# Performance work log

Measured on AMD Instinct MI355X. Metric: run time of the kernel, lower is better.

The kernel has to match this reference:

```python
import jax, jax.numpy as jnp
import numpy as np

N = 50000
E = 800000
D_IN = 64
D_HID = 64
N_CLASS = 40


def setup_inputs() -> dict:
    key = jax.random.key(0)
    ks = jax.random.split(key, 9)
    x = jax.random.normal(ks[0], (N, D_IN), dtype=jnp.float32)
    edge_index = jax.random.randint(ks[1], (2, E), 0, N, dtype=jnp.int64)
    # GCNConv weights (glorot-ish scale) and biases
    W1 = jax.random.normal(ks[2], (D_IN, D_HID), dtype=jnp.float32) / np.sqrt(D_IN)
    b1 = jnp.zeros((D_HID,), dtype=jnp.float32)
    W2 = jax.random.normal(ks[3], (D_HID, D_HID), dtype=jnp.float32) / np.sqrt(D_HID)
    b2 = jnp.zeros((D_HID,), dtype=jnp.float32)
    Wc = jax.random.normal(ks[4], (D_HID, N_CLASS), dtype=jnp.float32) / np.sqrt(D_HID)
    bc = jnp.zeros((N_CLASS,), dtype=jnp.float32)
    return {"x": x, "edge_index": edge_index, "W1": W1, "b1": b1,
            "W2": W2, "b2": b2, "Wc": Wc, "bc": bc}


def _gcn_conv(x, W, b, src, dst, n_nodes):
    """PyG GCNConv: add self-loops, sym-normalized mean aggregation, then +bias.
    out = D^{-1/2} (A + I) D^{-1/2} X W + b
    src/dst already include self-loops."""
    h = x @ W  # [N, D_out] -- transform before aggregation (fewer FLOPs if D_out<=D_in)
    deg = jax.ops.segment_sum(jnp.ones_like(dst, dtype=h.dtype), dst, num_segments=n_nodes)
    dinv = jnp.where(deg > 0, jax.lax.rsqrt(deg), 0.0)  # [N]
    norm = dinv[src] * dinv[dst]  # [E+N]
    msg = h[src] * norm[:, None]  # gather + scale
    out = jax.ops.segment_sum(msg, dst, num_segments=n_nodes)  # scatter-add
    return out + b


def reference(x, edge_index, W1, b1, W2, b2, Wc, bc):
    n = x.shape[0]
    loops = jnp.arange(n, dtype=edge_index.dtype)
    src = jnp.concatenate([edge_index[0], loops])
    dst = jnp.concatenate([edge_index[1], loops])
    h = jnp.tanh(_gcn_conv(x, W1, b1, src, dst, n))
    h = jnp.tanh(_gcn_conv(h, W2, b2, src, dst, n))
    out = h @ Wc + bc
    return (out, h)
```

## Files before the change

kernel.cpp:

```cpp
#include <hip/hip_runtime.h>
#include <math.h>

#define NN 50000
#define NE 800000
#define D 64
#define NC 40
#define NBUCK 196
#define SLAB 16384
#define EPB 2048
#define PADROW 0xC350C350u

typedef unsigned short u16;
typedef unsigned int u32;

__device__ __forceinline__ u16 f32_to_bf16(float v) {
    u32 x = __float_as_uint(v);
    x += 0x7FFFu + ((x >> 16) & 1u);
    return (u16)(x >> 16);
}
__device__ __forceinline__ float bflo(u32 v) { return __uint_as_float(v << 16); }
__device__ __forceinline__ float bfhi(u32 v) { return __uint_as_float(v & 0xffff0000u); }


__global__ __launch_bounds__(256) void bucket_scatter(const int* __restrict__ ei,
                                                      int* __restrict__ cursor,
                                                      u32* __restrict__ slab) {
    __shared__ int sums[256];
    __shared__ int lofs[256];
    __shared__ int lcur[256];
    __shared__ int gbase[256];
    __shared__ int tot_s;
    __shared__ u32 sorted[EPB];
    __shared__ int gdest[EPB];
    int tid = threadIdx.x;

    u32 pk[8];
    int nmine = 0;
    int e0 = blockIdx.x * EPB + tid * 8;
    if (e0 < NE) {
        nmine = 8;
#pragma unroll
        for (int j = 0; j < 2; ++j) {
            int4 ss = *(const int4*)&ei[e0 + j * 4];
            int4 dd = *(const int4*)&ei[NE + e0 + j * 4];
            pk[j * 4 + 0] = ((u32)dd.x << 16) | (u32)ss.x;
            pk[j * 4 + 1] = ((u32)dd.y << 16) | (u32)ss.y;
            pk[j * 4 + 2] = ((u32)dd.z << 16) | (u32)ss.z;
            pk[j * 4 + 3] = ((u32)dd.w << 16) | (u32)ss.w;
        }
    }

    sums[tid] = 0;
    __syncthreads();
    for (int j = 0; j < nmine; ++j) atomicAdd(&sums[pk[j] >> 24], 1);
    __syncthreads();
    int v = sums[tid];
    __syncthreads();
    for (int off = 1; off < 256; off <<= 1) {
        int u = (tid >= off) ? sums[tid - off] : 0;
        __syncthreads();
        sums[tid] += u;
        __syncthreads();
    }
    lofs[tid] = sums[tid] - v;
    lcur[tid] = sums[tid] - v;
    if (tid == 255) tot_s = sums[255];
    if (tid < NBUCK) gbase[tid] = atomicAdd(&cursor[tid], v);
    __syncthreads();

    for (int j = 0; j < nmine; ++j) {
        u32 p = pk[j];
        int bin = (int)(p >> 24);
        int pos = atomicAdd(&lcur[bin], 1);
        sorted[pos] = p;
        gdest[pos] = bin * SLAB + gbase[bin] + (pos - lofs[bin]);
    }
    __syncthreads();

    int tot = tot_s;
    for (int i = tid; i < tot; i += 256) slab[gdest[i]] = sorted[i];
}


__global__ __launch_bounds__(256) void ell_build(const u32* __restrict__ slab,
                                                 const int* __restrict__ cursor,
                                                 u16* __restrict__ ell,
                                                 int* __restrict__ cnt,
                                                 float* __restrict__ dinv) {
    __shared__ u16 ell_lds[256 * 64];
    __shared__ int cnt_lds[256];
    int b = blockIdx.x, tid = threadIdx.x;
    uint4* z = (uint4*)ell_lds;
    for (int i = tid; i < 2048; i += 256) z[i] = make_uint4(PADROW, PADROW, PADROW, PADROW);
    cnt_lds[tid] = 0;
    __syncthreads();

    int nE = cursor[b];
    const u32* run = slab + b * SLAB;
    int base = b * 256;
    for (int i = tid; i < nE; i += 256) {
        u32 p = run[i];
        int dl = (int)(p >> 16) - base;
        int r = atomicAdd(&cnt_lds[dl], 1);
        if (r < 64) ell_lds[dl * 64 + r] = (u16)(p & 0xffffu);
    }
    __syncthreads();

    int nNodes = NN - base; if (nNodes > 256) nNodes = 256;
    const uint4* s4 = (const uint4*)ell_lds;
    uint4* d4 = (uint4*)(ell + (size_t)base * 64);
    int n4 = nNodes * 8;
    for (int i = tid; i < n4; i += 256) d4[i] = s4[i];
    if (tid < nNodes) {
        int c = cnt_lds[tid];
        cnt[base + tid] = c;
        dinv[base + tid] = rsqrtf((float)c + 1.0f);
    }
}


__global__ __launch_bounds__(256) void gemm64_bf16(const float* __restrict__ A,
                                                   const float* __restrict__ W,
                                                   const float* __restrict__ dinv,
                                                   u16* __restrict__ C) {
    __shared__ float Ws[64 * 64];
    __shared__ __align__(16) float As[16 * 64];
    int tid = threadIdx.x;
    {
        const float4* w4 = (const float4*)W;
        float4* ws4 = (float4*)Ws;
#pragma unroll
        for (int j = 0; j < 4; ++j) ws4[tid + 256 * j] = w4[tid + 256 * j];
    }
    {
        const float4* a4 = (const float4*)(A + (size_t)blockIdx.x * 16 * 64);
        ((float4*)As)[tid] = a4[tid];
    }
    if (blockIdx.x == 0 && tid < 32) ((u32*)(C + (size_t)NN * 64))[tid] = 0u;
    __syncthreads();

    int r = tid >> 6, c = tid & 63;
    int rowBase = blockIdx.x * 16;
    float o0 = 0.f, o1 = 0.f, o2 = 0.f, o3 = 0.f;
#pragma unroll
    for (int k4 = 0; k4 < 16; ++k4) {
        float4 a0 = *(const float4*)&As[(r + 0) * 64 + k4 * 4];
        float4 a1 = *(const float4*)&As[(r + 4) * 64 + k4 * 4];
        float4 a2 = *(const float4*)&As[(r + 8) * 64 + k4 * 4];
        float4 a3 = *(const float4*)&As[(r + 12) * 64 + k4 * 4];
        float w0 = Ws[(k4 * 4 + 0) * 64 + c];
        float w1 = Ws[(k4 * 4 + 1) * 64 + c];
        float w2 = Ws[(k4 * 4 + 2) * 64 + c];
        float w3 = Ws[(k4 * 4 + 3) * 64 + c];
        o0 += a0.x * w0 + a0.y * w1 + a0.z * w2 + a0.w * w3;
        o1 += a1.x * w0 + a1.y * w1 + a1.z * w2 + a1.w * w3;
        o2 += a2.x * w0 + a2.y * w1 + a2.z * w2 + a2.w * w3;
        o3 += a3.x * w0 + a3.y * w1 + a3.z * w2 + a3.w * w3;
    }
    C[(size_t)(rowBase + r +  0) * 64 + c] = f32_to_bf16(o0 * dinv[rowBase + r +  0]);
    C[(size_t)(rowBase + r +  4) * 64 + c] = f32_to_bf16(o1 * dinv[rowBase + r +  4]);
    C[(size_t)(rowBase + r +  8) * 64 + c] = f32_to_bf16(o2 * dinv[rowBase + r +  8]);
    C[(size_t)(rowBase + r + 12) * 64 + c] = f32_to_bf16(o3 * dinv[rowBase + r + 12]);
}


__device__ __forceinline__ void gather_quad(const u16* __restrict__ ell,
                                            const int* __restrict__ cnt,
                                            const uint2* __restrict__ hs2,
                                            int base, int l,
                                            float& a0, float& a1, float& a2, float& a3) {
    int q = l >> 4, p = l & 15;
    int node = base + q;
    int4 c4 = *(const int4*)&cnt[base];
    int m01 = (c4.x > c4.y) ? c4.x : c4.y;
    int m23 = (c4.z > c4.w) ? c4.z : c4.w;
    int degmax = (m01 > m23) ? m01 : m23;
    if (degmax > 64) degmax = 64;

    uint2 iv = ((const uint2*)(ell + (size_t)node * 64))[p];

    uint2 sv = hs2[node * 16 + p];
    a0 = bflo(sv.x); a1 = bfhi(sv.x); a2 = bflo(sv.y); a3 = bfhi(sv.y);
    float e0 = 0.0f, e1 = 0.0f, e2 = 0.0f, e3 = 0.0f;

    for (int m = 0; m < degmax; m += 16) {
        uint2 st[16];
#pragma unroll
        for (int u = 0; u < 16; ++u) {
            u32 wsel = ((u >> 1) & 1) ? iv.y : iv.x;
            int bc = __shfl((int)wsel, (l & 48) + (m >> 2) + (u >> 2));
            int sid = (u & 1) ? (int)((u32)bc >> 16) : (int)(bc & 0xffff);
            st[u] = hs2[sid * 16 + p];
        }
#pragma unroll
        for (int u = 0; u < 16; ++u) {
            u32 x = st[u].x, y = st[u].y;
            if (u & 1) { e0 += bflo(x); e1 += bfhi(x); e2 += bflo(y); e3 += bfhi(y); }
            else       { a0 += bflo(x); a1 += bfhi(x); a2 += bflo(y); a3 += bfhi(y); }
        }
    }
    a0 += e0; a1 += e1; a2 += e2; a3 += e3;
}


__global__ __launch_bounds__(256) void gather_l1_fused(const u16* __restrict__ ell,
                                                       const int* __restrict__ cnt,
                                                       const u16* __restrict__ hs,
                                                       const float* __restrict__ dinv,
                                                       const float* __restrict__ b1,
                                                       const float* __restrict__ W2,
                                                       u16* __restrict__ hs_out) {
    __shared__ float Ws[64 * 64];
    __shared__ __align__(16) float hb[4][4][64];
    int tid = threadIdx.x;
    {
        const float4* w4 = (const float4*)W2;
        float4* ws4 = (float4*)Ws;
#pragma unroll
        for (int j = 0; j < 4; ++j) ws4[tid + 256 * j] = w4[tid + 256 * j];
    }
    if (blockIdx.x == 0 && tid < 32) ((u32*)(hs_out + (size_t)NN * 64))[tid] = 0u;

    int r = tid >> 6, l = tid & 63, q = l >> 4, p = l & 15;
    int base = (blockIdx.x * 4 + r) * 4;
    int node = base + q;

    float a0, a1, a2, a3;
    gather_quad(ell, cnt, (const uint2*)hs, base, l, a0, a1, a2, a3);

    float dv = dinv[node];
    float4 bb = *(const float4*)&b1[p * 4];
    float4 h = make_float4(tanhf(a0 * dv + bb.x), tanhf(a1 * dv + bb.y),
                           tanhf(a2 * dv + bb.z), tanhf(a3 * dv + bb.w));
    *(float4*)&hb[r][q][p * 4] = h;
    __syncthreads();

    int d = l;
    float4 dvv = *(const float4*)&dinv[base];
    float o0 = 0.0f, o1 = 0.0f, o2 = 0.0f, o3 = 0.0f;
#pragma unroll
    for (int k4 = 0; k4 < 16; ++k4) {
        float4 h0 = *(const float4*)&hb[r][0][k4 * 4];
        float4 h1 = *(const float4*)&hb[r][1][k4 * 4];
        float4 h2 = *(const float4*)&hb[r][2][k4 * 4];
        float4 h3 = *(const float4*)&hb[r][3][k4 * 4];
        float w0 = Ws[(k4 * 4 + 0) * 64 + d];
        float w1 = Ws[(k4 * 4 + 1) * 64 + d];
        float w2 = Ws[(k4 * 4 + 2) * 64 + d];
        float w3 = Ws[(k4 * 4 + 3) * 64 + d];
        o0 += h0.x * w0 + h0.y * w1 + h0.z * w2 + h0.w * w3;
        o1 += h1.x * w0 + h1.y * w1 + h1.z * w2 + h1.w * w3;
        o2 += h2.x * w0 + h2.y * w1 + h2.z * w2 + h2.w * w3;
        o3 += h3.x * w0 + h3.y * w1 + h3.z * w2 + h3.w * w3;
    }
    hs_out[(base + 0) * 64 + d] = f32_to_bf16(o0 * dvv.x);
    hs_out[(base + 1) * 64 + d] = f32_to_bf16(o1 * dvv.y);
    hs_out[(base + 2) * 64 + d] = f32_to_bf16(o2 * dvv.z);
    hs_out[(base + 3) * 64 + d] = f32_to_bf16(o3 * dvv.w);
}

__global__ __launch_bounds__(256) void gather_l2_fused(const u16* __restrict__ ell,
                                                       const int* __restrict__ cnt,
                                                       const u16* __restrict__ hs,
                                                       const float* __restrict__ dinv,
                                                       const float* __restrict__ b2,
                                                       const float* __restrict__ Wc,
                                                       const float* __restrict__ bc,
                                                       float* __restrict__ h_out,
                                                       float* __restrict__ out) {
    __shared__ float Ws[64 * NC];
    __shared__ float bs[NC];
    __shared__ __align__(16) float hb[4][4][64];
    int tid = threadIdx.x;
    for (int i = tid; i < 64 * NC; i += 256) Ws[i] = Wc[i];
    if (tid < NC) bs[tid] = bc[tid];

    int r = tid >> 6, l = tid & 63, q = l >> 4, p = l & 15;
    int base = (blockIdx.x * 4 + r) * 4;
    int node = base + q;

    float a0, a1, a2, a3;
    gather_quad(ell, cnt, (const uint2*)hs, base, l, a0, a1, a2, a3);

    float dv = dinv[node];
    float4 bb = *(const float4*)&b2[p * 4];
    float4 h = make_float4(tanhf(a0 * dv + bb.x), tanhf(a1 * dv + bb.y),
                           tanhf(a2 * dv + bb.z), tanhf(a3 * dv + bb.w));
    *(float4*)&h_out[node * 64 + p * 4] = h;
    *(float4*)&hb[r][q][p * 4] = h;
    __syncthreads();

    int d = l;
    int dc = (d < NC) ? d : NC - 1;
    float bcd = bs[dc];
    float o0 = bcd, o1 = bcd, o2 = bcd, o3 = bcd;
#pragma unroll
    for (int k4 = 0; k4 < 16; ++k4) {
        float4 v0 = *(const float4*)&hb[r][0][k4 * 4];
        float4 v1 = *(const float4*)&hb[r][1][k4 * 4];
        float4 v2 = *(const float4*)&hb[r][2][k4 * 4];
        float4 v3 = *(const float4*)&hb[r][3][k4 * 4];
        float w0 = Ws[(k4 * 4 + 0) * NC + dc];
        float w1 = Ws[(k4 * 4 + 1) * NC + dc];
        float w2 = Ws[(k4 * 4 + 2) * NC + dc];
        float w3 = Ws[(k4 * 4 + 3) * NC + dc];
        o0 += v0.x * w0 + v0.y * w1 + v0.z * w2 + v0.w * w3;
        o1 += v1.x * w0 + v1.y * w1 + v1.z * w2 + v1.w * w3;
        o2 += v2.x * w0 + v2.y * w1 + v2.z * w2 + v2.w * w3;
        o3 += v3.x * w0 + v3.y * w1 + v3.z * w2 + v3.w * w3;
    }
    if (d < NC) {
        out[(base + 0) * NC + d] = o0;
        out[(base + 1) * NC + d] = o1;
        out[(base + 2) * NC + d] = o2;
        out[(base + 3) * NC + d] = o3;
    }
}


extern "C" void kernel_launch(void* const* d_in, const int* in_sizes, int n_in,
                              void* d_out, int out_size, void* d_ws, size_t ws_size,
                              hipStream_t stream) {
    const float* x  = (const float*)d_in[0];
    const int*   ei = (const int*)d_in[1];
    const float* W1 = (const float*)d_in[2];
    const float* b1 = (const float*)d_in[3];
    const float* W2 = (const float*)d_in[4];
    const float* b2 = (const float*)d_in[5];
    const float* Wc = (const float*)d_in[6];
    const float* bc = (const float*)d_in[7];

    float* out   = (float*)d_out;
    float* h_out = out + NN * NC;

    u32*   slab   = (u32*)d_ws;
    int*   cursor = (int*)(slab + NBUCK * SLAB);
    int*   cnt    = cursor + 256;
    float* dinv   = (float*)(cnt + NN);
    u16*   ell    = (u16*)(dinv + NN);
    u16*   hsA    = ell + (size_t)NN * 64;
    u16*   hsB    = hsA + (size_t)(NN + 1) * 64;

    const int scatBlocks   = (NE + EPB - 1) / EPB;
    const int nodeBlocks16 = NN / 16;

    hipMemsetAsync(cursor, 0, NBUCK * sizeof(int), stream);
    bucket_scatter<<<scatBlocks, 256, 0, stream>>>(ei, cursor, slab);
    ell_build<<<NBUCK, 256, 0, stream>>>(slab, cursor, ell, cnt, dinv);

    gemm64_bf16<<<nodeBlocks16, 256, 0, stream>>>(x, W1, dinv, hsA);
    gather_l1_fused<<<nodeBlocks16, 256, 0, stream>>>(ell, cnt, hsA, dinv, b1, W2, hsB);
    gather_l2_fused<<<nodeBlocks16, 256, 0, stream>>>(ell, cnt, hsB, dinv, b2, Wc, bc,
                                                      h_out, out);
}
```

Measured before the change: 169.1 us.

## Split bf16 feature tables into column halves so gathers fit in cache

Stores each layer's bf16 feature table as two 32-column halves and runs each gather pass twice, once per half. Each pass works on a smaller random-access table (about 3.2 MB instead of 6.4 MB), which should improve cache hit rates for the random neighbor reads. The low half of the layer-1 activation is staged through an extra fp32 buffer, and the layer-2 low half is written to h_out and read back. This adds two kernel launches, re-reads the ELL structure for each half, and switches some stores to nontemporal.

```diff
diff --git a/kernel.cpp b/kernel.cpp
--- a/kernel.cpp
+++ b/kernel.cpp
@@ -122,7 +122,8 @@
 __global__ __launch_bounds__(256) void gemm64_bf16(const float* __restrict__ A,
                                                    const float* __restrict__ W,
                                                    const float* __restrict__ dinv,
-                                                   u16* __restrict__ C) {
+                                                   u16* __restrict__ Clo,
+                                                   u16* __restrict__ Chi) {
     __shared__ float Ws[64 * 64];
     __shared__ __align__(16) float As[16 * 64];
     int tid = threadIdx.x;
@@ -136,7 +137,8 @@
         const float4* a4 = (const float4*)(A + (size_t)blockIdx.x * 16 * 64);
         ((float4*)As)[tid] = a4[tid];
     }
-    if (blockIdx.x == 0 && tid < 32) ((u32*)(C + (size_t)NN * 64))[tid] = 0u;
+    if (blockIdx.x == 0 && tid < 16) ((u32*)(Clo + (size_t)NN * 32))[tid] = 0u;
+    if (blockIdx.x == 0 && tid >= 16 && tid < 32) ((u32*)(Chi + (size_t)NN * 32))[tid - 16] = 0u;
     __syncthreads();
 
     int r = tid >> 6, c = tid & 63;
@@ -157,18 +159,20 @@
         o2 += a2.x * w0 + a2.y * w1 + a2.z * w2 + a2.w * w3;
         o3 += a3.x * w0 + a3.y * w1 + a3.z * w2 + a3.w * w3;
     }
-    C[(size_t)(rowBase + r +  0) * 64 + c] = f32_to_bf16(o0 * dinv[rowBase + r +  0]);
-    C[(size_t)(rowBase + r +  4) * 64 + c] = f32_to_bf16(o1 * dinv[rowBase + r +  4]);
-    C[(size_t)(rowBase + r +  8) * 64 + c] = f32_to_bf16(o2 * dinv[rowBase + r +  8]);
-    C[(size_t)(rowBase + r + 12) * 64 + c] = f32_to_bf16(o3 * dinv[rowBase + r + 12]);
-}
-
-
-__device__ __forceinline__ void gather_quad(const u16* __restrict__ ell,
+    u16* Ch = (c < 32) ? Clo : Chi;
+    int cc = c & 31;
+    Ch[(size_t)(rowBase + r +  0) * 32 + cc] = f32_to_bf16(o0 * dinv[rowBase + r +  0]);
+    Ch[(size_t)(rowBase + r +  4) * 32 + cc] = f32_to_bf16(o1 * dinv[rowBase + r +  4]);
+    Ch[(size_t)(rowBase + r +  8) * 32 + cc] = f32_to_bf16(o2 * dinv[rowBase + r +  8]);
+    Ch[(size_t)(rowBase + r + 12) * 32 + cc] = f32_to_bf16(o3 * dinv[rowBase + r + 12]);
+}
+
+
+__device__ __forceinline__ void gather_half(const u16* __restrict__ ell,
                                             const int* __restrict__ cnt,
-                                            const uint2* __restrict__ hs2,
+                                            const u32* __restrict__ hsh,
                                             int base, int l,
-                                            float& a0, float& a1, float& a2, float& a3) {
+                                            float& a0, float& a1) {
     int q = l >> 4, p = l & 15;
     int node = base + q;
     int4 c4 = *(const int4*)&cnt[base];
@@ -179,37 +183,59 @@
 
     uint2 iv = ((const uint2*)(ell + (size_t)node * 64))[p];
 
-    uint2 sv = hs2[node * 16 + p];
-    a0 = bflo(sv.x); a1 = bfhi(sv.x); a2 = bflo(sv.y); a3 = bfhi(sv.y);
-    float e0 = 0.0f, e1 = 0.0f, e2 = 0.0f, e3 = 0.0f;
+    u32 sv = hsh[node * 16 + p];
+    a0 = bflo(sv); a1 = bfhi(sv);
+    float e0 = 0.0f, e1 = 0.0f;
 
     for (int m = 0; m < degmax; m += 16) {
-        uint2 st[16];
+        u32 st[16];
 #pragma unroll
         for (int u = 0; u < 16; ++u) {
             u32 wsel = ((u >> 1) & 1) ? iv.y : iv.x;
             int bc = __shfl((int)wsel, (l & 48) + (m >> 2) + (u >> 2));
             int sid = (u & 1) ? (int)((u32)bc >> 16) : (int)(bc & 0xffff);
-            st[u] = hs2[sid * 16 + p];
+            st[u] = hsh[sid * 16 + p];
         }
 #pragma unroll
         for (int u = 0; u < 16; ++u) {
-            u32 x = st[u].x, y = st[u].y;
-            if (u & 1) { e0 += bflo(x); e1 += bfhi(x); e2 += bflo(y); e3 += bfhi(y); }
-            else       { a0 += bflo(x); a1 += bfhi(x); a2 += bflo(y); a3 += bfhi(y); }
+            if (u & 1) { e0 += bflo(st[u]); e1 += bfhi(st[u]); }
+            else       { a0 += bflo(st[u]); a1 += bfhi(st[u]); }
         }
     }
-    a0 += e0; a1 += e1; a2 += e2; a3 += e3;
-}
-
-
-__global__ __launch_bounds__(256) void gather_l1_fused(const u16* __restrict__ ell,
-                                                       const int* __restrict__ cnt,
-                                                       const u16* __restrict__ hs,
-                                                       const float* __restrict__ dinv,
-                                                       const float* __restrict__ b1,
-                                                       const float* __restrict__ W2,
-                                                       u16* __restrict__ hs_out) {
+    a0 += e0; a1 += e1;
+}
+
+
+__global__ __launch_bounds__(256) void gather_l1_lo(const u16* __restrict__ ell,
+                                                    const int* __restrict__ cnt,
+                                                    const u32* __restrict__ hs_lo,
+                                                    const float* __restrict__ dinv,
+                                                    const float* __restrict__ b1,
+                                                    float* __restrict__ h1_lo) {
+    int tid = threadIdx.x;
+    int r = tid >> 6, l = tid & 63, q = l >> 4, p = l & 15;
+    int base = (blockIdx.x * 4 + r) * 4;
+    int node = base + q;
+
+    float a0, a1;
+    gather_half(ell, cnt, hs_lo, base, l, a0, a1);
+
+    float dv = dinv[node];
+    float2 bb = *(const float2*)&b1[p * 2];
+    float2 h = make_float2(tanhf(a0 * dv + bb.x), tanhf(a1 * dv + bb.y));
+    *(float2*)&h1_lo[(size_t)node * 32 + p * 2] = h;
+}
+
+
+__global__ __launch_bounds__(256) void gather_l1_hi(const u16* __restrict__ ell,
+                                                    const int* __restrict__ cnt,
+                                                    const u32* __restrict__ hs_hi,
+                                                    const float* __restrict__ h1_lo,
+                                                    const float* __restrict__ dinv,
+                                                    const float* __restrict__ b1,
+                                                    const float* __restrict__ W2,
+                                                    u16* __restrict__ hsB_lo,
+                                                    u16* __restrict__ hsB_hi) {
     __shared__ float Ws[64 * 64];
     __shared__ __align__(16) float hb[4][4][64];
     int tid = threadIdx.x;
@@ -219,20 +245,24 @@
 #pragma unroll
         for (int j = 0; j < 4; ++j) ws4[tid + 256 * j] = w4[tid + 256 * j];
     }
-    if (blockIdx.x == 0 && tid < 32) ((u32*)(hs_out + (size_t)NN * 64))[tid] = 0u;
+    if (blockIdx.x == 0 && tid < 16) ((u32*)(hsB_lo + (size_t)NN * 32))[tid] = 0u;
+    if (blockIdx.x == 0 && tid >= 16 && tid < 32) ((u32*)(hsB_hi + (size_t)NN * 32))[tid - 16] = 0u;
 
     int r = tid >> 6, l = tid & 63, q = l >> 4, p = l & 15;
     int base = (blockIdx.x * 4 + r) * 4;
     int node = base + q;
 
-    float a0, a1, a2, a3;
-    gather_quad(ell, cnt, (const uint2*)hs, base, l, a0, a1, a2, a3);
+    float a0, a1;
+    gather_half(ell, cnt, hs_hi, base, l, a0, a1);
 
     float dv = dinv[node];
-    float4 bb = *(const float4*)&b1[p * 4];
-    float4 h = make_float4(tanhf(a0 * dv + bb.x), tanhf(a1 * dv + bb.y),
-                           tanhf(a2 * dv + bb.z), tanhf(a3 * dv + bb.w));
-    *(float4*)&hb[r][q][p * 4] = h;
+    float2 bb = *(const float2*)&b1[32 + p * 2];
+    float2 h = make_float2(tanhf(a0 * dv + bb.x), tanhf(a1 * dv + bb.y));
+    *(float2*)&hb[r][q][32 + p * 2] = h;
+    {
+        float2 lo = *(const float2*)&h1_lo[(size_t)node * 32 + p * 2];
+        *(float2*)&hb[r][q][p * 2] = lo;
+    }
     __syncthreads();
 
     int d = l;
@@ -253,21 +283,45 @@
         o2 += h2.x * w0 + h2.y * w1 + h2.z * w2 + h2.w * w3;
         o3 += h3.x * w0 + h3.y * w1 + h3.z * w2 + h3.w * w3;
     }
-    hs_out[(base + 0) * 64 + d] = f32_to_bf16(o0 * dvv.x);
-    hs_out[(base + 1) * 64 + d] = f32_to_bf16(o1 * dvv.y);
-    hs_out[(base + 2) * 64 + d] = f32_to_bf16(o2 * dvv.z);
-    hs_out[(base + 3) * 64 + d] = f32_to_bf16(o3 * dvv.w);
-}
-
-__global__ __launch_bounds__(256) void gather_l2_fused(const u16* __restrict__ ell,
-                                                       const int* __restrict__ cnt,
-                                                       const u16* __restrict__ hs,
-                                                       const float* __restrict__ dinv,
-                                                       const float* __restrict__ b2,
-                                                       const float* __restrict__ Wc,
-                                                       const float* __restrict__ bc,
-                                                       float* __restrict__ h_out,
-                                                       float* __restrict__ out) {
+    u16* Bh = (d < 32) ? hsB_lo : hsB_hi;
+    int dd = d & 31;
+    __builtin_nontemporal_store(f32_to_bf16(o0 * dvv.x), &Bh[(size_t)(base + 0) * 32 + dd]);
+    __builtin_nontemporal_store(f32_to_bf16(o1 * dvv.y), &Bh[(size_t)(base + 1) * 32 + dd]);
+    __builtin_nontemporal_store(f32_to_bf16(o2 * dvv.z), &Bh[(size_t)(base + 2) * 32 + dd]);
+    __builtin_nontemporal_store(f32_to_bf16(o3 * dvv.w), &Bh[(size_t)(base + 3) * 32 + dd]);
+}
+
+
+__global__ __launch_bounds__(256) void gather_l2_lo(const u16* __restrict__ ell,
+                                                    const int* __restrict__ cnt,
+                                                    const u32* __restrict__ hsB_lo,
+                                                    const float* __restrict__ dinv,
+                                                    const float* __restrict__ b2,
+                                                    float* __restrict__ h_out) {
+    int tid = threadIdx.x;
+    int r = tid >> 6, l = tid & 63, q = l >> 4, p = l & 15;
+    int base = (blockIdx.x * 4 + r) * 4;
+    int node = base + q;
+
+    float a0, a1;
+    gather_half(ell, cnt, hsB_lo, base, l, a0, a1);
+
+    float dv = dinv[node];
+    float2 bb = *(const float2*)&b2[p * 2];
+    float2 h = make_float2(tanhf(a0 * dv + bb.x), tanhf(a1 * dv + bb.y));
+    *(float2*)&h_out[(size_t)node * 64 + p * 2] = h;
+}
+
+
+__global__ __launch_bounds__(256) void gather_l2_hi(const u16* __restrict__ ell,
+                                                    const int* __restrict__ cnt,
+                                                    const u32* __restrict__ hsB_hi,
+                                                    const float* __restrict__ dinv,
+                                                    const float* __restrict__ b2,
+                                                    const float* __restrict__ Wc,
+                                                    const float* __restrict__ bc,
+                                                    float* __restrict__ h_out,
+                                                    float* __restrict__ out) {
     __shared__ float Ws[64 * NC];
     __shared__ float bs[NC];
     __shared__ __align__(16) float hb[4][4][64];
@@ -279,15 +333,18 @@
     int base = (blockIdx.x * 4 + r) * 4;
     int node = base + q;
 
-    float a0, a1, a2, a3;
-    gather_quad(ell, cnt, (const uint2*)hs, base, l, a0, a1, a2, a3);
+    float a0, a1;
+    gather_half(ell, cnt, hsB_hi, base, l, a0, a1);
 
     float dv = dinv[node];
-    float4 bb = *(const float4*)&b2[p * 4];
-    float4 h = make_float4(tanhf(a0 * dv + bb.x), tanhf(a1 * dv + bb.y),
-                           tanhf(a2 * dv + bb.z), tanhf(a3 * dv + bb.w));
-    *(float4*)&h_out[node * 64 + p * 4] = h;
-    *(float4*)&hb[r][q][p * 4] = h;
+    float2 bb = *(const float2*)&b2[32 + p * 2];
+    float2 h = make_float2(tanhf(a0 * dv + bb.x), tanhf(a1 * dv + bb.y));
+    *(float2*)&h_out[(size_t)node * 64 + 32 + p * 2] = h;
+    *(float2*)&hb[r][q][32 + p * 2] = h;
+    {
+        float2 lo = *(const float2*)&h_out[(size_t)node * 64 + p * 2];
+        *(float2*)&hb[r][q][p * 2] = lo;
+    }
     __syncthreads();
 
     int d = l;
@@ -310,10 +367,10 @@
         o3 += v3.x * w0 + v3.y * w1 + v3.z * w2 + v3.w * w3;
     }
     if (d < NC) {
-        out[(base + 0) * NC + d] = o0;
-        out[(base + 1) * NC + d] = o1;
-        out[(base + 2) * NC + d] = o2;
-        out[(base + 3) * NC + d] = o3;
+        __builtin_nontemporal_store(o0, &out[(size_t)(base + 0) * NC + d]);
+        __builtin_nontemporal_store(o1, &out[(size_t)(base + 1) * NC + d]);
+        __builtin_nontemporal_store(o2, &out[(size_t)(base + 2) * NC + d]);
+        __builtin_nontemporal_store(o3, &out[(size_t)(base + 3) * NC + d]);
     }
 }
 
@@ -333,13 +390,16 @@
     float* out   = (float*)d_out;
     float* h_out = out + NN * NC;
 
-    u32*   slab   = (u32*)d_ws;
-    int*   cursor = (int*)(slab + NBUCK * SLAB);
-    int*   cnt    = cursor + 256;
-    float* dinv   = (float*)(cnt + NN);
-    u16*   ell    = (u16*)(dinv + NN);
-    u16*   hsA    = ell + (size_t)NN * 64;
-    u16*   hsB    = hsA + (size_t)(NN + 1) * 64;
+    u32*   slab    = (u32*)d_ws;
+    int*   cursor  = (int*)(slab + NBUCK * SLAB);
+    int*   cnt     = cursor + 256;
+    float* dinv    = (float*)(cnt + NN);
+    u16*   ell     = (u16*)(dinv + NN);
+    u16*   hsA_lo  = ell + (size_t)NN * 64;
+    u16*   hsA_hi  = hsA_lo + (size_t)(NN + 1) * 32;
+    u16*   hsB_lo  = hsA_hi + (size_t)(NN + 1) * 32;
+    u16*   hsB_hi  = hsB_lo + (size_t)(NN + 1) * 32;
+    float* h1_lo   = (float*)(hsB_hi + (size_t)(NN + 1) * 32);
 
     const int scatBlocks   = (NE + EPB - 1) / EPB;
     const int nodeBlocks16 = NN / 16;
@@ -348,8 +408,13 @@
     bucket_scatter<<<scatBlocks, 256, 0, stream>>>(ei, cursor, slab);
     ell_build<<<NBUCK, 256, 0, stream>>>(slab, cursor, ell, cnt, dinv);
 
-    gemm64_bf16<<<nodeBlocks16, 256, 0, stream>>>(x, W1, dinv, hsA);
-    gather_l1_fused<<<nodeBlocks16, 256, 0, stream>>>(ell, cnt, hsA, dinv, b1, W2, hsB);
-    gather_l2_fused<<<nodeBlocks16, 256, 0, stream>>>(ell, cnt, hsB, dinv, b2, Wc, bc,
-                                                      h_out, out);
-}
+    gemm64_bf16<<<nodeBlocks16, 256, 0, stream>>>(x, W1, dinv, hsA_lo, hsA_hi);
+
+    gather_l1_lo<<<nodeBlocks16, 256, 0, stream>>>(ell, cnt, (const u32*)hsA_lo, dinv, b1, h1_lo);
+    gather_l1_hi<<<nodeBlocks16, 256, 0, stream>>>(ell, cnt, (const u32*)hsA_hi, h1_lo, dinv,
+                                                   b1, W2, hsB_lo, hsB_hi);
+
+    gather_l2_lo<<<nodeBlocks16, 256, 0, stream>>>(ell, cnt, (const u32*)hsB_lo, dinv, b2, h_out);
+    gather_l2_hi<<<nodeBlocks16, 256, 0, stream>>>(ell, cnt, (const u32*)hsB_hi, dinv, b2,
+                                                   Wc, bc, h_out, out);
+}
```

After: 180.3 us. 1.07x slower.
